# Kernel tuning notes

Measured on AMD Instinct MI355X. Metric: run time of the kernel, lower is better.

## Reference

```python
import jax, jax.numpy as jnp
import numpy as np


def _ccl(x, w, b):
    # FFT-domain circular conv: rfft2 -> complex multiply + sum over c_in -> irfft2 + bias
    H, W = x.shape[-2], x.shape[-1]
    xf = jnp.fft.rfft2(x)                 # [B, Ci, H, Wf] complex
    wf = jnp.fft.rfft2(w, s=(H, W))       # [Co, Ci, H, Wf] complex
    hf = jnp.einsum('bihw,oihw->bohw', xf, wf)
    return jnp.fft.irfft2(hf, s=(H, W)) + b[:, None, None]


def _maxpool(x, ph, pw):
    B, C, H, W = x.shape
    return x.reshape(B, C, H // ph, ph, W // pw, pw).max(axis=(3, 5))


def _upsample_zero(x, sh, sw):
    B, C, H, W = x.shape
    y = jnp.zeros((B, C, H * sh, W * sw), dtype=x.dtype)
    return y.at[:, :, ::sh, ::sw].set(x)


def setup_inputs() -> dict:
    key = jax.random.key(0)
    ks = jax.random.split(key, 11)
    inp = {"x": jax.random.normal(ks[0], (16, 2, 64, 256), dtype=jnp.float32)}
    specs = [  # (c_out, c_in, kh, kw)
        (50, 1, 3, 7), (50, 50, 3, 7), (50, 50, 3, 5), (50, 50, 3, 7), (1, 50, 3, 7)]
    for i, (co, ci, kh, kw) in enumerate(specs):
        K = float(np.sqrt(1.0 / (ci * kh * kw)))
        inp[f"w{i+1}"] = (2 * jax.random.uniform(ks[2 * i + 1], (co, ci, kh, kw), dtype=jnp.float32) - 1) * K
        inp[f"b{i+1}"] = (2 * jax.random.uniform(ks[2 * i + 2], (co,), dtype=jnp.float32) - 1) * K
    return inp


def reference(x, w1, b1, w2, b2, w3, b3, w4, b4, w5, b5):
    H, W = x.shape[-2], x.shape[-1]
    h = x.reshape(-1, 1, H, W)                       # [2B, 1, 64, 256]
    h = jax.nn.relu(_maxpool(_ccl(h, w1, b1), 2, 4))  # [2B, 50, 32, 64]
    h = jax.nn.relu(_maxpool(_ccl(h, w2, b2), 2, 4))  # [2B, 50, 16, 16]
    h = h.reshape(-1, 2, h.shape[-3], h.shape[-2], h.shape[-1])
    h = h[:, 0] + h[:, 1].mean(axis=(-1, -2))[..., None, None]  # [B, 50, 16, 16]
    h = jax.nn.relu(_ccl(_upsample_zero(h, 2, 4), w3, b3))       # [B, 50, 32, 64]
    h = jax.nn.relu(_ccl(_upsample_zero(h, 2, 4), w4, b4))       # [B, 50, 64, 256]
    h = jax.nn.sigmoid(_ccl(h, w5, b5))                          # [B, 1, 64, 256]
    return h.squeeze(1)
```

## Files before the change

### kernel.cpp

```cpp
#include <hip/hip_runtime.h>
#include <math.h>

__global__ void kprep(const float* __restrict__ w2, const float* __restrict__ w3,
                      const float* __restrict__ w4, float* __restrict__ w2t,
                      float* __restrict__ w3t, float* __restrict__ w4t) {
  int i = blockIdx.x * 256 + threadIdx.x;
  if (i < 52500) {
    int co = i % 50, r = i / 50;
    w2t[i] = w2[co * 1050 + r];
    w4t[i] = w4[co * 1050 + r];
  } else {
    int j = i - 52500;
    if (j < 37500) {
      int co = j % 50, r = j / 50;
      w3t[j] = w3[co * 750 + r];
    }
  }
}

__global__ __launch_bounds__(256) void k1(const float* __restrict__ x,
                                          const float* __restrict__ w1,
                                          const float* __restrict__ b1,
                                          float* __restrict__ a1) {
  int b = blockIdx.z;
  int pr0 = blockIdx.x * 4;
  int co0 = blockIdx.y * 10;
  int ty = threadIdx.x >> 6;
  int pc = threadIdx.x & 63;
  int pr = pr0 + ty;
  const float* xb = x + b * (64 * 256);
  float xw[4][10];
#pragma unroll
  for (int r = 0; r < 4; ++r) {
    int row = (2 * pr - 2 + r) & 63;
#pragma unroll
    for (int c = 0; c < 10; ++c) {
      int col = (4 * pc - 6 + c) & 255;
      xw[r][c] = xb[row * 256 + col];
    }
  }
#pragma unroll
  for (int cq = 0; cq < 10; ++cq) {
    int co = co0 + cq;
    const float* wp = w1 + co * 21;
    float m = -1e30f;
#pragma unroll
    for (int iy = 0; iy < 2; ++iy) {
#pragma unroll
      for (int jx = 0; jx < 4; ++jx) {
        float s = 0.f;
#pragma unroll
        for (int di = 0; di < 3; ++di)
#pragma unroll
          for (int dj = 0; dj < 7; ++dj)
            s = fmaf(xw[iy + 2 - di][jx + 6 - dj], wp[di * 7 + dj], s);
        m = fmaxf(m, s);
      }
    }
    float v = fmaxf(m + b1[co], 0.f);
    a1[((b * 50 + co) * 32 + pr) * 64 + pc] = v;
  }
}

__global__ __launch_bounds__(256) void k2(const float* __restrict__ a1,
                                          const float* __restrict__ w2t,
                                          const float* __restrict__ b2,
                                          float* __restrict__ a2) {
  __shared__ float sm[3840];
  int b = blockIdx.z;
  int r0 = blockIdx.x * 4;
  int cc = blockIdx.y;
  int co0 = cc * 10;
  int y = threadIdx.x >> 6;
  int xcol = threadIdx.x & 63;
  float acc[10];
#pragma unroll
  for (int co = 0; co < 10; ++co) acc[co] = b2[co0 + co];
  const float* ain = a1 + b * (50 * 2048);
  for (int cci = 0; cci < 5; ++cci) {
    __syncthreads();
    for (int e = threadIdx.x; e < 3840; e += 256) {
      int ci = e / 384;
      int rr = (e >> 6) % 6;
      int col = e & 63;
      int row = (r0 - 2 + rr) & 31;
      sm[e] = ain[(cci * 10 + ci) * 2048 + row * 64 + col];
    }
    __syncthreads();
    for (int ci = 0; ci < 10; ++ci) {
      const float* sin_ = sm + ci * 384;
      const float* wbase = w2t + (cci * 10 + ci) * 21 * 50 + co0;
#pragma unroll
      for (int di = 0; di < 3; ++di) {
        const float* srow = sin_ + (y + 2 - di) * 64;
#pragma unroll
        for (int dj = 0; dj < 7; ++dj) {
          float xv = srow[(xcol - dj) & 63];
          const float* wrow = wbase + (di * 7 + dj) * 50;
#pragma unroll
          for (int co = 0; co < 10; ++co)
            acc[co] = fmaf(xv, wrow[co], acc[co]);
        }
      }
    }
  }
  __syncthreads();
#pragma unroll
  for (int k = 0; k < 10; ++k)
    sm[k * 256 + y * 64 + xcol] = acc[k];
  __syncthreads();
  for (int w = threadIdx.x; w < 320; w += 256) {
    int cop = w / 32;
    int pr = (w >> 4) & 1;
    int pc = w & 15;
    float m = -1e30f;
#pragma unroll
    for (int yy = 0; yy < 2; ++yy)
#pragma unroll
      for (int xx = 0; xx < 4; ++xx)
        m = fmaxf(m, sm[cop * 256 + (pr * 2 + yy) * 64 + pc * 4 + xx]);
    m = fmaxf(m, 0.f);
    a2[((b * 50 + co0 + cop) * 16 + (r0 >> 1) + pr) * 16 + pc] = m;
  }
}

__global__ __launch_bounds__(512) void k3(const float* __restrict__ a2,
                                          const float* __restrict__ w3t,
                                          const float* __restrict__ b3,
                                          float* __restrict__ a3) {
  __shared__ float ts[4000];
  __shared__ float mean_s[64];
  __shared__ float part[200];
  int b = blockIdx.z;
  int r0 = blockIdx.x * 8;
  int co0 = blockIdx.y * 10;
  int tid = threadIdx.x;
  const float* aodd = a2 + (2 * b + 1) * (50 * 256);
  if (tid < 200) {
    int ci = tid >> 2, p = tid & 3;
    float s = 0.f;
    for (int k = 0; k < 64; ++k) s += aodd[ci * 256 + p * 64 + k];
    part[tid] = s;
  }
  __syncthreads();
  if (tid < 50)
    mean_s[tid] = (part[4 * tid] + part[4 * tid + 1] + part[4 * tid + 2] + part[4 * tid + 3]) * (1.f / 256.f);
  __syncthreads();
  const float* aev = a2 + (2 * b) * (50 * 256);
  for (int e = tid; e < 4000; e += 512) {
    int ci = e / 80;
    int rr = (e >> 4) % 5;
    int tc = e & 15;
    int trow = ((r0 >> 1) - 1 + rr) & 15;
    ts[e] = aev[ci * 256 + trow * 16 + tc] + mean_s[ci];
  }
  __syncthreads();
  int wv = __builtin_amdgcn_readfirstlane(tid >> 6);
  int lane = tid & 63;
  int p = wv >> 2;
  int m = wv & 3;
  int q = lane & 15;
  int yidx = lane >> 4;
  int i = r0 + 2 * yidx + p;
  int j = 4 * q + m;
  float acc[10];
#pragma unroll
  for (int co = 0; co < 10; ++co) acc[co] = b3[co0 + co];
  int ndi = (p == 0) ? 2 : 1;
  int ndj = (m == 0) ? 2 : 1;
  for (int aa = 0; aa < ndi; ++aa) {
    int di = (p == 0) ? (2 * aa) : 1;
    int rr = 1 + ((2 * yidx + p - di) >> 1);
    for (int e2 = 0; e2 < ndj; ++e2) {
      int dj = (m == 0) ? (4 * e2) : m;
      int tc = ((j - dj + 64) >> 2) & 15;
      for (int ci = 0; ci < 50; ++ci) {
        float xv = ts[ci * 80 + rr * 16 + tc];
        const float* wrow = w3t + (ci * 15 + di * 5 + dj) * 50 + co0;
#pragma unroll
        for (int co = 0; co < 10; ++co)
          acc[co] = fmaf(xv, wrow[co], acc[co]);
      }
    }
  }
  float* aout = a3 + b * (50 * 2048);
#pragma unroll
  for (int co = 0; co < 10; ++co)
    aout[(co0 + co) * 2048 + i * 64 + j] = fmaxf(acc[co], 0.f);
}

__global__ __launch_bounds__(512) void k4(const float* __restrict__ a3,
                                          const float* __restrict__ w4t,
                                          const float* __restrict__ b4,
                                          float* __restrict__ a4) {
  __shared__ float s4[6400];
  int b = blockIdx.z;
  int r0 = blockIdx.x * 2;
  int co0 = blockIdx.y * 10;
  int tid = threadIdx.x;
  const float* ain = a3 + b * (50 * 2048);
  for (int e = tid; e < 6400; e += 512) {
    int ci = e >> 7;
    int rr = (e >> 6) & 1;
    int col = e & 63;
    int row = ((r0 >> 1) - 1 + rr) & 31;
    s4[e] = ain[ci * 2048 + row * 64 + col];
  }
  __syncthreads();
  int wv = __builtin_amdgcn_readfirstlane(tid >> 6);
  int lane = tid & 63;
  int rowsel = wv >> 2;
  int m = wv & 3;
  int i = r0 + rowsel;
  int j = 4 * lane + m;
  float acc[10];
#pragma unroll
  for (int co = 0; co < 10; ++co) acc[co] = b4[co0 + co];
  int ndi = (rowsel == 0) ? 2 : 1;
  int ndj = (m < 3) ? 2 : 1;
  for (int aa = 0; aa < ndi; ++aa) {
    int di = (rowsel == 0) ? (2 * aa) : 1;
    int rr = 1 - (di >> 1);
    for (int e2 = 0; e2 < ndj; ++e2) {
      int dj = m + 4 * e2;
      int tc = ((j - dj) >> 2) & 63;
      for (int ci = 0; ci < 50; ++ci) {
        float xv = s4[ci * 128 + rr * 64 + tc];
        const float* wrow = w4t + (ci * 21 + di * 7 + dj) * 50 + co0;
#pragma unroll
        for (int co = 0; co < 10; ++co)
          acc[co] = fmaf(xv, wrow[co], acc[co]);
      }
    }
  }
  float* aout = a4 + b * (50 * 16384);
#pragma unroll
  for (int co = 0; co < 10; ++co)
    aout[(co0 + co) * 16384 + i * 256 + j] = fmaxf(acc[co], 0.f);
}

__global__ __launch_bounds__(256) void k5(const float* __restrict__ a4,
                                          const float* __restrict__ w5,
                                          const float* __restrict__ b5,
                                          float* __restrict__ out) {
  __shared__ __align__(16) float s5[7920];
  int bid = blockIdx.x;
  int b = bid >> 4;
  int r0 = (bid & 15) * 4;
  int tid = threadIdx.x;
  int y = tid >> 6;
  int q = tid & 63;
  int j0 = q * 4;
  float acc0 = b5[0], acc1 = b5[0], acc2 = b5[0], acc3 = b5[0];
  const float* ain = a4 + b * (50 * 16384);
  for (int cc = 0; cc < 10; ++cc) {
    __syncthreads();
    for (int e = tid; e < 7920; e += 256) {
      int ci = e / 1584;
      int rr = (e / 264) % 6;
      int c = e % 264;
      int row = (r0 - 2 + rr) & 63;
      int col = (c - 8) & 255;
      s5[e] = ain[(cc * 5 + ci) * 16384 + row * 256 + col];
    }
    __syncthreads();
#pragma unroll
    for (int ci = 0; ci < 5; ++ci) {
#pragma unroll
      for (int di = 0; di < 3; ++di) {
        const float4* prow = (const float4*)&s5[ci * 1584 + (y + 2 - di) * 264 + j0];
        float4 v0 = prow[0], v1 = prow[1], v2 = prow[2];
        float wnd[12] = {v0.x, v0.y, v0.z, v0.w, v1.x, v1.y, v1.z, v1.w,
                         v2.x, v2.y, v2.z, v2.w};
        const float* wp = w5 + ((cc * 5 + ci) * 3 + di) * 7;
#pragma unroll
        for (int dj = 0; dj < 7; ++dj) {
          float wgt = wp[dj];
          acc0 = fmaf(wnd[8 - dj], wgt, acc0);
          acc1 = fmaf(wnd[9 - dj], wgt, acc1);
          acc2 = fmaf(wnd[10 - dj], wgt, acc2);
          acc3 = fmaf(wnd[11 - dj], wgt, acc3);
        }
      }
    }
  }
  float4 r;
  r.x = 1.f / (1.f + expf(-acc0));
  r.y = 1.f / (1.f + expf(-acc1));
  r.z = 1.f / (1.f + expf(-acc2));
  r.w = 1.f / (1.f + expf(-acc3));
  *(float4*)(out + b * 16384 + (r0 + y) * 256 + j0) = r;
}

extern "C" void kernel_launch(void* const* d_in, const int* in_sizes, int n_in,
                              void* d_out, int out_size, void* d_ws, size_t ws_size,
                              hipStream_t stream) {
  (void)in_sizes; (void)n_in; (void)out_size; (void)ws_size;
  const float* x  = (const float*)d_in[0];
  const float* w1 = (const float*)d_in[1];
  const float* b1 = (const float*)d_in[2];
  const float* w2 = (const float*)d_in[3];
  const float* b2 = (const float*)d_in[4];
  const float* w3 = (const float*)d_in[5];
  const float* b3 = (const float*)d_in[6];
  const float* w4 = (const float*)d_in[7];
  const float* b4 = (const float*)d_in[8];
  const float* w5 = (const float*)d_in[9];
  const float* b5 = (const float*)d_in[10];
  float* out = (float*)d_out;
  float* ws  = (float*)d_ws;
  float* w2t = ws;
  float* w3t = w2t + 52500;
  float* w4t = w3t + 37500;
  float* a1  = w4t + 52500;
  float* a2  = a1 + 32 * 50 * 32 * 64;
  float* a3  = a2 + 32 * 50 * 16 * 16;
  float* a4  = a3 + 16 * 50 * 32 * 64;
  hipLaunchKernelGGL(kprep, dim3(352), dim3(256), 0, stream, w2, w3, w4, w2t, w3t, w4t);
  hipLaunchKernelGGL(k1, dim3(8, 5, 32), dim3(256), 0, stream, x, w1, b1, a1);
  hipLaunchKernelGGL(k2, dim3(8, 5, 32), dim3(256), 0, stream, a1, w2t, b2, a2);
  hipLaunchKernelGGL(k3, dim3(4, 5, 16), dim3(512), 0, stream, a2, w3t, b3, a3);
  hipLaunchKernelGGL(k4, dim3(32, 5, 16), dim3(512), 0, stream, a3, w4t, b4, a4);
  hipLaunchKernelGGL(k5, dim3(256), dim3(256), 0, stream, a4, w5, b5, out);
}
```

Measured before the change: 368.1 us.

## Register-block k2 conv over 4 columns and 5 channels with float4 smem loads

Reworks the layer-2 circular conv kernel so each thread computes a 4-column by 5-output-channel tile, loading a 12-element sliding window from shared memory with float4 reads and reusing each weight across 4 pixels. Blocks now cover 16 rows and 5 output channels (grid 2x10x32), staging 18 halo rows per input channel with vectorized global loads. Maxpool is done in registers plus a cross-lane shuffle instead of a shared-memory round trip. This cuts shared-memory and weight-load traffic per FMA, at the cost of more registers and fewer blocks.

After: 371.1 us. No clear change (+0.8%).

```diff
diff --git a/kernel.cpp b/kernel.cpp
--- a/kernel.cpp
+++ b/kernel.cpp
@@ -66,61 +66,66 @@
                                           const float* __restrict__ w2t,
                                           const float* __restrict__ b2,
                                           float* __restrict__ a2) {
-  __shared__ float sm[3840];
+  __shared__ __align__(16) float sm[10 * 18 * 64];
   int b = blockIdx.z;
-  int r0 = blockIdx.x * 4;
-  int cc = blockIdx.y;
-  int co0 = cc * 10;
-  int y = threadIdx.x >> 6;
-  int xcol = threadIdx.x & 63;
-  float acc[10];
-#pragma unroll
-  for (int co = 0; co < 10; ++co) acc[co] = b2[co0 + co];
+  int r0 = blockIdx.x * 16;
+  int co0 = blockIdx.y * 5;
+  int tid = threadIdx.x;
+  int y = tid >> 4;
+  int g = tid & 15;
+  float acc[5][4];
+#pragma unroll
+  for (int co = 0; co < 5; ++co) {
+    float bc = b2[co0 + co];
+#pragma unroll
+    for (int cc = 0; cc < 4; ++cc) acc[co][cc] = bc;
+  }
   const float* ain = a1 + b * (50 * 2048);
   for (int cci = 0; cci < 5; ++cci) {
     __syncthreads();
-    for (int e = threadIdx.x; e < 3840; e += 256) {
-      int ci = e / 384;
-      int rr = (e >> 6) % 6;
-      int col = e & 63;
+    for (int e = tid; e < 2880; e += 256) {
+      int ci = e / 288;
+      int rem = e - ci * 288;
+      int rr = rem >> 4;
+      int c4 = rem & 15;
       int row = (r0 - 2 + rr) & 31;
-      sm[e] = ain[(cci * 10 + ci) * 2048 + row * 64 + col];
+      *(float4*)&sm[(ci * 18 + rr) * 64 + c4 * 4] =
+          *(const float4*)&ain[(cci * 10 + ci) * 2048 + row * 64 + c4 * 4];
     }
     __syncthreads();
     for (int ci = 0; ci < 10; ++ci) {
-      const float* sin_ = sm + ci * 384;
-      const float* wbase = w2t + (cci * 10 + ci) * 21 * 50 + co0;
-#pragma unroll
-      for (int di = 0; di < 3; ++di) {
-        const float* srow = sin_ + (y + 2 - di) * 64;
+      const float* sbase = sm + ci * 1152 + y * 64;
+      const float* wci = w2t + (cci * 10 + ci) * 1050 + co0;
+#pragma unroll
+      for (int dr = 0; dr < 3; ++dr) {
+        const float* rp = sbase + dr * 64;
+        float4 v0 = *(const float4*)&rp[(4 * g - 8) & 63];
+        float4 v1 = *(const float4*)&rp[(4 * g - 4) & 63];
+        float4 v2 = *(const float4*)&rp[4 * g];
+        float win[12] = {v0.x, v0.y, v0.z, v0.w, v1.x, v1.y, v1.z, v1.w,
+                         v2.x, v2.y, v2.z, v2.w};
+        const float* wr = wci + (2 - dr) * 350;
 #pragma unroll
         for (int dj = 0; dj < 7; ++dj) {
-          float xv = srow[(xcol - dj) & 63];
-          const float* wrow = wbase + (di * 7 + dj) * 50;
-#pragma unroll
-          for (int co = 0; co < 10; ++co)
-            acc[co] = fmaf(xv, wrow[co], acc[co]);
+          const float* wp = wr + dj * 50;
+#pragma unroll
+          for (int co = 0; co < 5; ++co) {
+            float wgt = wp[co];
+#pragma unroll
+            for (int cc = 0; cc < 4; ++cc)
+              acc[co][cc] = fmaf(win[8 + cc - dj], wgt, acc[co][cc]);
+          }
         }
       }
     }
   }
-  __syncthreads();
-#pragma unroll
-  for (int k = 0; k < 10; ++k)
-    sm[k * 256 + y * 64 + xcol] = acc[k];
-  __syncthreads();
-  for (int w = threadIdx.x; w < 320; w += 256) {
-    int cop = w / 32;
-    int pr = (w >> 4) & 1;
-    int pc = w & 15;
-    float m = -1e30f;
-#pragma unroll
-    for (int yy = 0; yy < 2; ++yy)
-#pragma unroll
-      for (int xx = 0; xx < 4; ++xx)
-        m = fmaxf(m, sm[cop * 256 + (pr * 2 + yy) * 64 + pc * 4 + xx]);
-    m = fmaxf(m, 0.f);
-    a2[((b * 50 + co0 + cop) * 16 + (r0 >> 1) + pr) * 16 + pc] = m;
+#pragma unroll
+  for (int co = 0; co < 5; ++co) {
+    float m = fmaxf(fmaxf(acc[co][0], acc[co][1]), fmaxf(acc[co][2], acc[co][3]));
+    float o = fmaxf(m, __shfl_xor(m, 16));
+    o = fmaxf(o, 0.f);
+    if (!(y & 1))
+      a2[((b * 50 + co0 + co) * 16 + ((r0 + y) >> 1)) * 16 + g] = o;
   }
 }
 
@@ -318,7 +323,7 @@
   float* a4  = a3 + 16 * 50 * 32 * 64;
   hipLaunchKernelGGL(kprep, dim3(352), dim3(256), 0, stream, w2, w3, w4, w2t, w3t, w4t);
   hipLaunchKernelGGL(k1, dim3(8, 5, 32), dim3(256), 0, stream, x, w1, b1, a1);
-  hipLaunchKernelGGL(k2, dim3(8, 5, 32), dim3(256), 0, stream, a1, w2t, b2, a2);
+  hipLaunchKernelGGL(k2, dim3(2, 10, 32), dim3(256), 0, stream, a1, w2t, b2, a2);
   hipLaunchKernelGGL(k3, dim3(4, 5, 16), dim3(512), 0, stream, a2, w3t, b3, a3);
   hipLaunchKernelGGL(k4, dim3(32, 5, 16), dim3(512), 0, stream, a3, w4t, b4, a4);
   hipLaunchKernelGGL(k5, dim3(256), dim3(256), 0, stream, a4, w5, b5, out);
```
